# Kernel optimization log

Hardware: AMD Instinct MI355X
Metric: run time of the kernel (lower is better)

## Reference

```python
import jax, jax.numpy as jnp
import numpy as np

DEPTH = 3
DIM = 64
N_NODES = 4096
BATCH = 4


def setup_inputs() -> dict:
    key = jax.random.key(0)
    k1, k2, k3, k4 = jax.random.split(key, 4)
    x = jax.random.normal(k1, (BATCH, N_NODES, DIM), dtype=jnp.float32)
    graph = jax.random.uniform(k2, (BATCH, N_NODES, N_NODES), dtype=jnp.float32)
    # Linear((depth+1)*dim, dim): PyTorch default init U(-1/sqrt(fan_in), 1/sqrt(fan_in))
    fan_in = (DEPTH + 1) * DIM
    bound = 1.0 / np.sqrt(fan_in)
    W = jax.random.uniform(k3, (DIM, fan_in), minval=-bound, maxval=bound, dtype=jnp.float32)
    b = jax.random.uniform(k4, (DIM,), minval=-bound, maxval=bound, dtype=jnp.float32)
    return {"x": x, "graph": graph, "W": W, "b": b}


def reference(x, graph, W, b):
    # GCN branch of LocalGNN.forward (dropout p=0 -> identity).
    n = graph.shape[-1]
    g = graph + jnp.eye(n, dtype=graph.dtype)          # add self loops
    d = 1.0 / (jnp.sqrt(g.sum(axis=-1)) + 1e-7)        # [b, n]
    # D @ g @ D with D = diag(d):  g_ij * d_i * d_j
    g = g * d[..., :, None] * d[..., None, :]
    outs = [x]
    h = x
    for _ in range(DEPTH):
        h = jnp.einsum('bij,bjd->bid', g, h)           # dense propagation
        outs.append(h)
    cat = jnp.concatenate(outs, axis=-1)               # [b, n, (depth+1)*dim]
    return cat @ W.T + b
```

## Files before the change

### kernel.cpp

```cpp
#include <hip/hip_runtime.h>
#include <hip/hip_bf16.h>


typedef __attribute__((ext_vector_type(4))) float  floatx4;
typedef __attribute__((ext_vector_type(8))) short  short8;

#define NB 4
#define NN 4096
#define ND 64
#define HSZ ((size_t)NB * NN * ND)
#define HF_B 262144

__device__ __forceinline__ unsigned short f2bf_bits(float v) {
    __hip_bfloat16 b = __float2bfloat16(v);
    return *reinterpret_cast<unsigned short*>(&b);
}

__device__ __forceinline__ short8 pack8p(const float* v) {
    short8 r;
#pragma unroll
    for (int j = 0; j < 8; ++j) r[j] = (short)f2bf_bits(v[j]);
    return r;
}

__global__ void rowsum_kernel(const float* __restrict__ graph, float* __restrict__ dinv) {
    int row = blockIdx.x;
    const float* g = graph + (size_t)row * NN;
    int t = threadIdx.x;
    float s = 0.f;
#pragma unroll
    for (int q = 0; q < 4; ++q) {
        floatx4 v = *reinterpret_cast<const floatx4*>(g + q * 1024 + t * 4);
        s += v[0] + v[1] + v[2] + v[3];
    }
#pragma unroll
    for (int off = 32; off > 0; off >>= 1) s += __shfl_down(s, off);
    __shared__ float wsum[4];
    if ((t & 63) == 0) wsum[t >> 6] = s;
    __syncthreads();
    if (t == 0) {
        float tot = wsum[0] + wsum[1] + wsum[2] + wsum[3] + 1.0f;
        dinv[row] = 1.0f / (sqrtf(tot) + 1e-7f);
    }
}

__global__ __launch_bounds__(256) void make_ghat_sw(const float* __restrict__ g,
                                                    const float* __restrict__ dinv,
                                                    unsigned short* __restrict__ gsw) {
    __shared__ float tile[16][524];
    int bid = blockIdx.x;
    int b = bid >> 8, mt = bid & 255;
    int t = threadIdx.x;
    const float* grow  = g + ((size_t)b * NN + mt * 16) * NN;
    const float* dinvb = dinv + (size_t)b * NN;
    size_t outbase = (((size_t)(b * 256 + mt)) * 128) * 512;

    for (int s0 = 0; s0 < NN; s0 += 512) {
        __syncthreads();
#pragma unroll
        for (int li = 0; li < 8; ++li) {
            int flat = li * 1024 + t * 4;
            int r = flat >> 9, cidx = flat & 511;
            floatx4 v = *reinterpret_cast<const floatx4*>(grow + (size_t)r * NN + s0 + cidx);
            *reinterpret_cast<floatx4*>(&tile[r][cidx]) = v;
        }
        __syncthreads();
#pragma unroll
        for (int gg = 0; gg < 4; ++gg) {
            int gi = gg * 256 + t;
            int kcl = gi >> 6;
            int ln  = gi & 63;
            int m = ln & 15, q = ln >> 4;
            int i_row = mt * 16 + m;
            float di = dinvb[i_row];
            int kbase = s0 + kcl * 32 + q * 8;
            floatx4 dj0 = *reinterpret_cast<const floatx4*>(dinvb + kbase);
            floatx4 dj1 = *reinterpret_cast<const floatx4*>(dinvb + kbase + 4);
            float v[8];
#pragma unroll
            for (int j = 0; j < 8; ++j) {
                float xv = tile[m][kcl * 32 + q * 8 + j];
                if (kbase + j == i_row) xv += 1.0f;
                float dj = (j < 4) ? dj0[j] : dj1[j - 4];
                v[j] = xv * di * dj;
            }
            short8 o = pack8p(v);
            size_t kc = (size_t)(s0 >> 5) + kcl;
            *reinterpret_cast<short8*>(gsw + outbase + kc * 512 + ln * 8) = o;
        }
    }
}

__global__ void castF_kernel(const float* __restrict__ x, unsigned short* __restrict__ hF) {
    __shared__ float tile[64][65];
    int b = blockIdx.y, row0 = blockIdx.x * 64;
    size_t base = ((size_t)b * NN + row0) * ND;
    int t = threadIdx.x;
#pragma unroll
    for (int qi = 0; qi < 16; ++qi) {
        int idx = qi * 256 + t;
        tile[idx >> 6][idx & 63] = x[base + idx];
    }
    __syncthreads();
#pragma unroll
    for (int gg = 0; gg < 2; ++gg) {
        int gi = gg * 256 + t;
        int kcl = gi >> 8;
        int c   = (gi >> 6) & 3;
        int ln  = gi & 63;
        int m = ln & 15, q = ln >> 4;
        float v[8];
#pragma unroll
        for (int j = 0; j < 8; ++j) v[j] = tile[kcl * 32 + q * 8 + j][c * 16 + m];
        short8 o = pack8p(v);
        size_t kc = (size_t)blockIdx.x * 2 + kcl;
        *reinterpret_cast<short8*>(hF + (size_t)b * HF_B + ((kc * 4 + c) * 64 + ln) * 8) = o;
    }
}

__global__ __launch_bounds__(256, 4) void prop_gemm(const unsigned short* __restrict__ gsw,
                                                    const unsigned short* __restrict__ hF,
                                                    float* __restrict__ P) {
    int wid  = blockIdx.x * 4 + (threadIdx.x >> 6);
    int lane = threadIdx.x & 63;
    int b  = wid >> 10;
    int ks = (wid >> 8) & 3;
    int mt = wid & 255;
    int m = lane & 15, q = lane >> 4;

    const unsigned short* Ap = gsw + (((size_t)(b * 256 + mt)) * 128 + ks * 32) * 512 + lane * 8;
    const unsigned short* Bp = hF + (size_t)b * HF_B + (size_t)(ks * 32) * 2048 + lane * 8;

    floatx4 acc0 = {0.f,0.f,0.f,0.f}, acc1 = acc0, acc2 = acc0, acc3 = acc0;

#pragma unroll 2
    for (int kc = 0; kc < 32; ++kc) {
        short8 a  = *reinterpret_cast<const short8*>(Ap);
        short8 b0 = *reinterpret_cast<const short8*>(Bp);
        short8 b1 = *reinterpret_cast<const short8*>(Bp + 512);
        short8 b2 = *reinterpret_cast<const short8*>(Bp + 1024);
        short8 b3 = *reinterpret_cast<const short8*>(Bp + 1536);
        Ap += 512;
        Bp += 2048;
        acc0 = __builtin_amdgcn_mfma_f32_16x16x32_bf16(a, b0, acc0, 0, 0, 0);
        acc1 = __builtin_amdgcn_mfma_f32_16x16x32_bf16(a, b1, acc1, 0, 0, 0);
        acc2 = __builtin_amdgcn_mfma_f32_16x16x32_bf16(a, b2, acc2, 0, 0, 0);
        acc3 = __builtin_amdgcn_mfma_f32_16x16x32_bf16(a, b3, acc3, 0, 0, 0);
    }

    float* pout = P + ((size_t)ks * NB + b) * ((size_t)NN * ND);
    int row0 = mt * 16;
    floatx4* accs[4] = {&acc0, &acc1, &acc2, &acc3};
#pragma unroll
    for (int c = 0; c < 4; ++c)
#pragma unroll
        for (int r = 0; r < 4; ++r) {
            int row = row0 + q * 4 + r;
            pout[(size_t)row * ND + c * 16 + m] = (*accs[c])[r];
        }
}

__global__ void prep_kernel(const float* __restrict__ P,
                            unsigned short* __restrict__ hrow,
                            unsigned short* __restrict__ hF) {
    __shared__ float tile[64][65];
    int b = blockIdx.y, row0 = blockIdx.x * 64;
    size_t base = ((size_t)b * NN + row0) * ND;
    const size_t SZ = HSZ;
    int t = threadIdx.x;
#pragma unroll
    for (int qi = 0; qi < 16; ++qi) {
        int idx = qi * 256 + t;
        int r = idx >> 6, n = idx & 63;
        size_t off = base + idx;
        float s = P[off] + P[SZ + off] + P[2 * SZ + off] + P[3 * SZ + off];
        hrow[off] = f2bf_bits(s);
        tile[r][n] = s;
    }
    __syncthreads();
#pragma unroll
    for (int gg = 0; gg < 2; ++gg) {
        int gi = gg * 256 + t;
        int kcl = gi >> 8;
        int c   = (gi >> 6) & 3;
        int ln  = gi & 63;
        int m = ln & 15, q = ln >> 4;
        float v[8];
#pragma unroll
        for (int j = 0; j < 8; ++j) v[j] = tile[kcl * 32 + q * 8 + j][c * 16 + m];
        short8 o = pack8p(v);
        size_t kc = (size_t)blockIdx.x * 2 + kcl;
        *reinterpret_cast<short8*>(hF + (size_t)b * HF_B + ((kc * 4 + c) * 64 + ln) * 8) = o;
    }
}

__global__ __launch_bounds__(256) void final_linear(const float* __restrict__ x,
                                                    const unsigned short* __restrict__ h1,
                                                    const unsigned short* __restrict__ h2,
                                                    const unsigned short* __restrict__ h3,
                                                    const float* __restrict__ W,
                                                    const float* __restrict__ bias,
                                                    float* __restrict__ out) {
    int wid  = blockIdx.x * 4 + (threadIdx.x >> 6);
    int lane = threadIdx.x & 63;
    int b = wid >> 8;
    int row0 = (wid & 255) * 16;
    int m = lane & 15, q = lane >> 4;

    floatx4 acc[4];
#pragma unroll
    for (int c = 0; c < 4; ++c) acc[c] = (floatx4){0.f, 0.f, 0.f, 0.f};

    {
        const float* A = x + ((size_t)b * NN + row0 + m) * ND;
#pragma unroll
        for (int ki = 0; ki < 2; ++ki) {
            float av[8];
#pragma unroll
            for (int j = 0; j < 8; ++j) av[j] = A[ki * 32 + q * 8 + j];
            short8 af = pack8p(av);
#pragma unroll
            for (int c = 0; c < 4; ++c) {
                const float* Wr = W + (size_t)(c * 16 + m) * 256 + ki * 32 + q * 8;
                float wv[8];
#pragma unroll
                for (int j = 0; j < 8; ++j) wv[j] = Wr[j];
                short8 bf = pack8p(wv);
                acc[c] = __builtin_amdgcn_mfma_f32_16x16x32_bf16(af, bf, acc[c], 0, 0, 0);
            }
        }
    }
    const unsigned short* hs[3] = {h1, h2, h3};
#pragma unroll
    for (int p = 1; p < 4; ++p) {
        const unsigned short* A = hs[p - 1] + ((size_t)b * NN + row0 + m) * ND;
#pragma unroll
        for (int ki = 0; ki < 2; ++ki) {
            short8 af = *reinterpret_cast<const short8*>(A + ki * 32 + q * 8);
#pragma unroll
            for (int c = 0; c < 4; ++c) {
                const float* Wr = W + (size_t)(c * 16 + m) * 256 + p * 64 + ki * 32 + q * 8;
                float wv[8];
#pragma unroll
                for (int j = 0; j < 8; ++j) wv[j] = Wr[j];
                short8 bf = pack8p(wv);
                acc[c] = __builtin_amdgcn_mfma_f32_16x16x32_bf16(af, bf, acc[c], 0, 0, 0);
            }
        }
    }
#pragma unroll
    for (int c = 0; c < 4; ++c) {
        float bb = bias[c * 16 + m];
#pragma unroll
        for (int r = 0; r < 4; ++r) {
            int row = row0 + q * 4 + r;
            out[((size_t)b * NN + row) * ND + c * 16 + m] = acc[c][r] + bb;
        }
    }
}

extern "C" void kernel_launch(void* const* d_in, const int* in_sizes, int n_in,
                              void* d_out, int out_size, void* d_ws, size_t ws_size,
                              hipStream_t stream) {
    const float* x     = (const float*)d_in[0];
    const float* graph = (const float*)d_in[1];
    const float* W     = (const float*)d_in[2];
    const float* bias  = (const float*)d_in[3];
    float* out = (float*)d_out;

    char* w = (char*)d_ws;
    float*          dinv = (float*)w;
    unsigned short* hF   = (unsigned short*)(w + (1 << 16));
    unsigned short* gsw  = (unsigned short*)(w + (1 << 16) + (1 << 21));
    char* w2 = w + (1 << 16) + (1 << 21) + ((size_t)NB * NN * NN * 2);
    float*          P    = (float*)w2;
    unsigned short* h1   = (unsigned short*)(w2 + 4 * HSZ * 4);
    unsigned short* h2   = h1 + HSZ;
    unsigned short* h3   = h2 + HSZ;

    rowsum_kernel<<<NB * NN, 256, 0, stream>>>(graph, dinv);
    make_ghat_sw<<<NB * 256, 256, 0, stream>>>(graph, dinv, gsw);
    castF_kernel<<<dim3(NN / 64, NB), 256, 0, stream>>>(x, hF);

    unsigned short* houts[3] = {h1, h2, h3};
    for (int s = 0; s < 3; ++s) {
        prop_gemm<<<1024, 256, 0, stream>>>(gsw, hF, P);
        prep_kernel<<<dim3(NN / 64, NB), 256, 0, stream>>>(P, houts[s], hF);
    }
    final_linear<<<256, 256, 0, stream>>>(x, h1, h2, h3, W, bias, out);
}
```

Measured before the change: 591.4 us.

## Fuse rowsum into graph prep, apply D scaling to features, fuse split-K reduction and final linear

Rowsum and graph swizzling are merged into one pass that reads the graph once, storing the unnormalised (g+I) in bf16 and folding the D^-1/2 scaling onto the feature vectors instead. The propagation GEMM now reduces its split-K partials in shared memory within a block and writes bf16 outputs directly, removing the fp32 partial buffer and the separate prep kernels. The last propagation is fused with the final linear layer, and W is pre-swizzled to bf16 once. Kernel count drops from nine to four, at the cost of fewer blocks per GEMM launch and extra shared-memory syncs.

Measured after the change: 498.5 us. 1.19x faster.

```diff
diff --git a/kernel.cpp b/kernel.cpp
--- a/kernel.cpp
+++ b/kernel.cpp
@@ -8,14 +8,16 @@
 #define NB 4
 #define NN 4096
 #define ND 64
-#define HSZ ((size_t)NB * NN * ND)
 #define HF_B 262144
 
 __device__ __forceinline__ unsigned short f2bf_bits(float v) {
     __hip_bfloat16 b = __float2bfloat16(v);
     return *reinterpret_cast<unsigned short*>(&b);
 }
-
+__device__ __forceinline__ float bf2f(unsigned short u) {
+    unsigned int x = ((unsigned int)u) << 16;
+    return *reinterpret_cast<float*>(&x);
+}
 __device__ __forceinline__ short8 pack8p(const float* v) {
     short8 r;
 #pragma unroll
@@ -23,238 +25,239 @@
     return r;
 }
 
-__global__ void rowsum_kernel(const float* __restrict__ graph, float* __restrict__ dinv) {
-    int row = blockIdx.x;
-    const float* g = graph + (size_t)row * NN;
+__global__ __launch_bounds__(256) void prep_graph(const float* __restrict__ g,
+                                                  const float* __restrict__ x,
+                                                  const float* __restrict__ W,
+                                                  float* __restrict__ dinv,
+                                                  unsigned short* __restrict__ gswz,
+                                                  unsigned short* __restrict__ hF0,
+                                                  unsigned short* __restrict__ Wf) {
+    __shared__ float tile[16][516];
+    __shared__ float dl[16];
+    int tt = blockIdx.x;
+    int b = tt >> 8, mt = tt & 255;
     int t = threadIdx.x;
-    float s = 0.f;
-#pragma unroll
-    for (int q = 0; q < 4; ++q) {
-        floatx4 v = *reinterpret_cast<const floatx4*>(g + q * 1024 + t * 4);
-        s += v[0] + v[1] + v[2] + v[3];
-    }
-#pragma unroll
-    for (int off = 32; off > 0; off >>= 1) s += __shfl_down(s, off);
-    __shared__ float wsum[4];
-    if ((t & 63) == 0) wsum[t >> 6] = s;
-    __syncthreads();
-    if (t == 0) {
-        float tot = wsum[0] + wsum[1] + wsum[2] + wsum[3] + 1.0f;
-        dinv[row] = 1.0f / (sqrtf(tot) + 1e-7f);
-    }
-}
-
-__global__ __launch_bounds__(256) void make_ghat_sw(const float* __restrict__ g,
-                                                    const float* __restrict__ dinv,
-                                                    unsigned short* __restrict__ gsw) {
-    __shared__ float tile[16][524];
-    int bid = blockIdx.x;
-    int b = bid >> 8, mt = bid & 255;
-    int t = threadIdx.x;
-    const float* grow  = g + ((size_t)b * NN + mt * 16) * NN;
-    const float* dinvb = dinv + (size_t)b * NN;
-    size_t outbase = (((size_t)(b * 256 + mt)) * 128) * 512;
+    const float* grow = g + ((size_t)b * NN + mt * 16) * NN;
+    size_t outbase = (size_t)tt * 128 * 512;
+    float rs = 0.f;
 
     for (int s0 = 0; s0 < NN; s0 += 512) {
         __syncthreads();
 #pragma unroll
-        for (int li = 0; li < 8; ++li) {
-            int flat = li * 1024 + t * 4;
-            int r = flat >> 9, cidx = flat & 511;
-            floatx4 v = *reinterpret_cast<const floatx4*>(grow + (size_t)r * NN + s0 + cidx);
-            *reinterpret_cast<floatx4*>(&tile[r][cidx]) = v;
+        for (int it = 0; it < 8; ++it) {
+            int f4 = it * 256 + t;
+            int r = f4 >> 7, c4 = f4 & 127;
+            floatx4 v = *reinterpret_cast<const floatx4*>(grow + (size_t)r * NN + s0 + c4 * 4);
+            *reinterpret_cast<floatx4*>(&tile[r][c4 * 4]) = v;
         }
         __syncthreads();
+        {
+            int r = t >> 4, c0 = t & 15;
+            float s = 0.f;
+#pragma unroll
+            for (int j2 = 0; j2 < 32; ++j2) s += tile[r][c0 + j2 * 16];
+            rs += s;
+        }
 #pragma unroll
         for (int gg = 0; gg < 4; ++gg) {
             int gi = gg * 256 + t;
             int kcl = gi >> 6;
-            int ln  = gi & 63;
+            int ln = gi & 63;
             int m = ln & 15, q = ln >> 4;
             int i_row = mt * 16 + m;
-            float di = dinvb[i_row];
             int kbase = s0 + kcl * 32 + q * 8;
-            floatx4 dj0 = *reinterpret_cast<const floatx4*>(dinvb + kbase);
-            floatx4 dj1 = *reinterpret_cast<const floatx4*>(dinvb + kbase + 4);
             float v[8];
 #pragma unroll
             for (int j = 0; j < 8; ++j) {
                 float xv = tile[m][kcl * 32 + q * 8 + j];
                 if (kbase + j == i_row) xv += 1.0f;
-                float dj = (j < 4) ? dj0[j] : dj1[j - 4];
-                v[j] = xv * di * dj;
+                v[j] = xv;
             }
-            short8 o = pack8p(v);
-            size_t kc = (size_t)(s0 >> 5) + kcl;
-            *reinterpret_cast<short8*>(gsw + outbase + kc * 512 + ln * 8) = o;
-        }
-    }
-}
-
-__global__ void castF_kernel(const float* __restrict__ x, unsigned short* __restrict__ hF) {
-    __shared__ float tile[64][65];
-    int b = blockIdx.y, row0 = blockIdx.x * 64;
-    size_t base = ((size_t)b * NN + row0) * ND;
-    int t = threadIdx.x;
-#pragma unroll
-    for (int qi = 0; qi < 16; ++qi) {
-        int idx = qi * 256 + t;
-        tile[idx >> 6][idx & 63] = x[base + idx];
+            *reinterpret_cast<short8*>(gswz + outbase + ((size_t)((s0 >> 5) + kcl)) * 512 + ln * 8) = pack8p(v);
+        }
+    }
+#pragma unroll
+    for (int off = 8; off > 0; off >>= 1) rs += __shfl_down(rs, off, 16);
+    if ((t & 15) == 0) {
+        int r = t >> 4;
+        float d = 1.0f / (sqrtf(rs + 1.0f) + 1e-7f);
+        dinv[b * NN + mt * 16 + r] = d;
+        dl[r] = d;
     }
     __syncthreads();
-#pragma unroll
-    for (int gg = 0; gg < 2; ++gg) {
-        int gi = gg * 256 + t;
-        int kcl = gi >> 8;
-        int c   = (gi >> 6) & 3;
-        int ln  = gi & 63;
-        int m = ln & 15, q = ln >> 4;
+    {
+        const float* xp = x + ((size_t)b * NN + mt * 16) * ND;
+#pragma unroll
+        for (int e = 0; e < 4; ++e) {
+            int idx = e * 256 + t;
+            tile[idx >> 6][idx & 63] = xp[idx];
+        }
+    }
+    __syncthreads();
+    if (t < 128) {
+        int c = t >> 5, lnl = t & 31;
+        int q_loc = lnl >> 4, m = lnl & 15;
+        int u = mt & 1;
+        int ln = u * 32 + lnl;
+        int kc = mt >> 1;
         float v[8];
 #pragma unroll
-        for (int j = 0; j < 8; ++j) v[j] = tile[kcl * 32 + q * 8 + j][c * 16 + m];
-        short8 o = pack8p(v);
-        size_t kc = (size_t)blockIdx.x * 2 + kcl;
-        *reinterpret_cast<short8*>(hF + (size_t)b * HF_B + ((kc * 4 + c) * 64 + ln) * 8) = o;
-    }
-}
-
-__global__ __launch_bounds__(256, 4) void prop_gemm(const unsigned short* __restrict__ gsw,
-                                                    const unsigned short* __restrict__ hF,
-                                                    float* __restrict__ P) {
-    int wid  = blockIdx.x * 4 + (threadIdx.x >> 6);
-    int lane = threadIdx.x & 63;
-    int b  = wid >> 10;
-    int ks = (wid >> 8) & 3;
-    int mt = wid & 255;
-    int m = lane & 15, q = lane >> 4;
-
-    const unsigned short* Ap = gsw + (((size_t)(b * 256 + mt)) * 128 + ks * 32) * 512 + lane * 8;
-    const unsigned short* Bp = hF + (size_t)b * HF_B + (size_t)(ks * 32) * 2048 + lane * 8;
-
-    floatx4 acc0 = {0.f,0.f,0.f,0.f}, acc1 = acc0, acc2 = acc0, acc3 = acc0;
-
-#pragma unroll 2
-    for (int kc = 0; kc < 32; ++kc) {
-        short8 a  = *reinterpret_cast<const short8*>(Ap);
-        short8 b0 = *reinterpret_cast<const short8*>(Bp);
-        short8 b1 = *reinterpret_cast<const short8*>(Bp + 512);
-        short8 b2 = *reinterpret_cast<const short8*>(Bp + 1024);
-        short8 b3 = *reinterpret_cast<const short8*>(Bp + 1536);
-        Ap += 512;
-        Bp += 2048;
-        acc0 = __builtin_amdgcn_mfma_f32_16x16x32_bf16(a, b0, acc0, 0, 0, 0);
-        acc1 = __builtin_amdgcn_mfma_f32_16x16x32_bf16(a, b1, acc1, 0, 0, 0);
-        acc2 = __builtin_amdgcn_mfma_f32_16x16x32_bf16(a, b2, acc2, 0, 0, 0);
-        acc3 = __builtin_amdgcn_mfma_f32_16x16x32_bf16(a, b3, acc3, 0, 0, 0);
-    }
-
-    float* pout = P + ((size_t)ks * NB + b) * ((size_t)NN * ND);
-    int row0 = mt * 16;
-    floatx4* accs[4] = {&acc0, &acc1, &acc2, &acc3};
-#pragma unroll
-    for (int c = 0; c < 4; ++c)
-#pragma unroll
-        for (int r = 0; r < 4; ++r) {
-            int row = row0 + q * 4 + r;
-            pout[(size_t)row * ND + c * 16 + m] = (*accs[c])[r];
-        }
-}
-
-__global__ void prep_kernel(const float* __restrict__ P,
-                            unsigned short* __restrict__ hrow,
-                            unsigned short* __restrict__ hF) {
-    __shared__ float tile[64][65];
-    int b = blockIdx.y, row0 = blockIdx.x * 64;
-    size_t base = ((size_t)b * NN + row0) * ND;
-    const size_t SZ = HSZ;
-    int t = threadIdx.x;
-#pragma unroll
-    for (int qi = 0; qi < 16; ++qi) {
-        int idx = qi * 256 + t;
-        int r = idx >> 6, n = idx & 63;
-        size_t off = base + idx;
-        float s = P[off] + P[SZ + off] + P[2 * SZ + off] + P[3 * SZ + off];
-        hrow[off] = f2bf_bits(s);
-        tile[r][n] = s;
-    }
+        for (int j = 0; j < 8; ++j) {
+            int lr = q_loc * 8 + j;
+            v[j] = dl[lr] * tile[lr][c * 16 + m];
+        }
+        *reinterpret_cast<short8*>(hF0 + (size_t)b * HF_B + ((size_t)(kc * 4 + c) * 64 + ln) * 8) = pack8p(v);
+    }
+    if (tt == 0) {
+#pragma unroll
+        for (int e = 0; e < 8; ++e) {
+            int wi = e * 256 + t;
+            int kc = wi >> 8;
+            int c = (wi >> 6) & 3;
+            int ln = wi & 63;
+            int m = ln & 15, q = ln >> 4;
+            float v[8];
+#pragma unroll
+            for (int j = 0; j < 8; ++j) v[j] = W[(size_t)(c * 16 + m) * 256 + kc * 32 + q * 8 + j];
+            *reinterpret_cast<short8*>(Wf + ((size_t)(kc * 4 + c) * 64 + ln) * 8) = pack8p(v);
+        }
+    }
+}
+
+#define PROP_MAIN()                                                                      \
+    int bid = blockIdx.x;                                                                \
+    int b = bid >> 7, mk = bid & 127;                                                    \
+    int t = threadIdx.x;                                                                 \
+    int w = t >> 6, lane = t & 63;                                                       \
+    int m = lane & 15, q = lane >> 4;                                                    \
+    int tt0 = b * 256 + mk * 2;                                                          \
+    const unsigned short* Ap0 = gswz + ((size_t)tt0 * 128 + w * 32) * 512 + lane * 8;    \
+    const unsigned short* Ap1 = Ap0 + (size_t)128 * 512;                                 \
+    const unsigned short* Bp  = hFin + (size_t)b * HF_B + (size_t)(w * 32) * 2048 + lane * 8; \
+    floatx4 acc0[4], acc1[4];                                                            \
+    _Pragma("unroll")                                                                    \
+    for (int c = 0; c < 4; ++c) { acc0[c] = (floatx4){0.f,0.f,0.f,0.f}; acc1[c] = acc0[c]; } \
+    _Pragma("unroll 2")                                                                  \
+    for (int kc = 0; kc < 32; ++kc) {                                                    \
+        short8 a0 = *reinterpret_cast<const short8*>(Ap0);                               \
+        short8 a1 = *reinterpret_cast<const short8*>(Ap1);                               \
+        short8 b0 = *reinterpret_cast<const short8*>(Bp);                                \
+        short8 b1 = *reinterpret_cast<const short8*>(Bp + 512);                          \
+        short8 b2 = *reinterpret_cast<const short8*>(Bp + 1024);                         \
+        short8 b3 = *reinterpret_cast<const short8*>(Bp + 1536);                         \
+        Ap0 += 512; Ap1 += 512; Bp += 2048;                                              \
+        acc0[0] = __builtin_amdgcn_mfma_f32_16x16x32_bf16(a0, b0, acc0[0], 0, 0, 0);     \
+        acc1[0] = __builtin_amdgcn_mfma_f32_16x16x32_bf16(a1, b0, acc1[0], 0, 0, 0);     \
+        acc0[1] = __builtin_amdgcn_mfma_f32_16x16x32_bf16(a0, b1, acc0[1], 0, 0, 0);     \
+        acc1[1] = __builtin_amdgcn_mfma_f32_16x16x32_bf16(a1, b1, acc1[1], 0, 0, 0);     \
+        acc0[2] = __builtin_amdgcn_mfma_f32_16x16x32_bf16(a0, b2, acc0[2], 0, 0, 0);     \
+        acc1[2] = __builtin_amdgcn_mfma_f32_16x16x32_bf16(a1, b2, acc1[2], 0, 0, 0);     \
+        acc0[3] = __builtin_amdgcn_mfma_f32_16x16x32_bf16(a0, b3, acc0[3], 0, 0, 0);     \
+        acc1[3] = __builtin_amdgcn_mfma_f32_16x16x32_bf16(a1, b3, acc1[3], 0, 0, 0);     \
+    }                                                                                    \
+    if (t < 32) dl[t] = dinv[b * NN + mk * 32 + t];                                      \
+    for (int u = 0; u < 2; ++u) {                                                        \
+        __syncthreads();                                                                 \
+        floatx4* acc = u ? acc1 : acc0;                                                  \
+        _Pragma("unroll")                                                                \
+        for (int c = 0; c < 4; ++c)                                                      \
+            _Pragma("unroll")                                                            \
+            for (int r = 0; r < 4; ++r) buf[w][q * 4 + r][c * 16 + m] = acc[c][r];       \
+        __syncthreads();                                                                 \
+        _Pragma("unroll")                                                                \
+        for (int e = 0; e < 4; ++e) {                                                    \
+            int idx = e * 256 + t;                                                       \
+            int r = idx >> 6, col = idx & 63;                                            \
+            float s = buf[0][r][col] + buf[1][r][col] + buf[2][r][col] + buf[3][r][col]; \
+            int lr = u * 16 + r;                                                         \
+            hsh[lr][col] = f2bf_bits(dl[lr] * s);                                        \
+        }                                                                                \
+    }                                                                                    \
     __syncthreads();
-#pragma unroll
-    for (int gg = 0; gg < 2; ++gg) {
-        int gi = gg * 256 + t;
-        int kcl = gi >> 8;
-        int c   = (gi >> 6) & 3;
-        int ln  = gi & 63;
-        int m = ln & 15, q = ln >> 4;
+
+__global__ __launch_bounds__(256) void prop_pass(const unsigned short* __restrict__ gswz,
+                                                 const unsigned short* __restrict__ hFin,
+                                                 const float* __restrict__ dinv,
+                                                 unsigned short* __restrict__ hrow,
+                                                 unsigned short* __restrict__ hFout) {
+    __shared__ float buf[4][16][68];
+    __shared__ unsigned short hsh[32][64];
+    __shared__ float dl[32];
+    PROP_MAIN()
+    {
+        unsigned short* hp = hrow + ((size_t)b * NN + mk * 32) * ND;
+#pragma unroll
+        for (int e = 0; e < 8; ++e) {
+            int idx = e * 256 + t;
+            hp[idx] = hsh[idx >> 6][idx & 63];
+        }
+    }
+    {
+        int c = t >> 6, ln = t & 63;
+        int mm = ln & 15, qq = ln >> 4;
         float v[8];
 #pragma unroll
-        for (int j = 0; j < 8; ++j) v[j] = tile[kcl * 32 + q * 8 + j][c * 16 + m];
-        short8 o = pack8p(v);
-        size_t kc = (size_t)blockIdx.x * 2 + kcl;
-        *reinterpret_cast<short8*>(hF + (size_t)b * HF_B + ((kc * 4 + c) * 64 + ln) * 8) = o;
-    }
-}
-
-__global__ __launch_bounds__(256) void final_linear(const float* __restrict__ x,
-                                                    const unsigned short* __restrict__ h1,
-                                                    const unsigned short* __restrict__ h2,
-                                                    const unsigned short* __restrict__ h3,
-                                                    const float* __restrict__ W,
-                                                    const float* __restrict__ bias,
-                                                    float* __restrict__ out) {
-    int wid  = blockIdx.x * 4 + (threadIdx.x >> 6);
-    int lane = threadIdx.x & 63;
-    int b = wid >> 8;
-    int row0 = (wid & 255) * 16;
-    int m = lane & 15, q = lane >> 4;
-
-    floatx4 acc[4];
-#pragma unroll
-    for (int c = 0; c < 4; ++c) acc[c] = (floatx4){0.f, 0.f, 0.f, 0.f};
-
-    {
-        const float* A = x + ((size_t)b * NN + row0 + m) * ND;
-#pragma unroll
-        for (int ki = 0; ki < 2; ++ki) {
-            float av[8];
-#pragma unroll
-            for (int j = 0; j < 8; ++j) av[j] = A[ki * 32 + q * 8 + j];
-            short8 af = pack8p(av);
-#pragma unroll
-            for (int c = 0; c < 4; ++c) {
-                const float* Wr = W + (size_t)(c * 16 + m) * 256 + ki * 32 + q * 8;
-                float wv[8];
-#pragma unroll
-                for (int j = 0; j < 8; ++j) wv[j] = Wr[j];
-                short8 bf = pack8p(wv);
-                acc[c] = __builtin_amdgcn_mfma_f32_16x16x32_bf16(af, bf, acc[c], 0, 0, 0);
+        for (int j = 0; j < 8; ++j) {
+            int lr = qq * 8 + j;
+            v[j] = dl[lr] * bf2f(hsh[lr][c * 16 + mm]);
+        }
+        *reinterpret_cast<short8*>(hFout + (size_t)b * HF_B + ((size_t)(mk * 4 + c) * 64 + ln) * 8) = pack8p(v);
+    }
+}
+
+__global__ __launch_bounds__(256) void prop_final(const unsigned short* __restrict__ gswz,
+                                                  const unsigned short* __restrict__ hFin,
+                                                  const float* __restrict__ dinv,
+                                                  const float* __restrict__ x,
+                                                  const unsigned short* __restrict__ hrow1,
+                                                  const unsigned short* __restrict__ hrow2,
+                                                  const unsigned short* __restrict__ Wf,
+                                                  const float* __restrict__ bias,
+                                                  float* __restrict__ out) {
+    __shared__ float buf[4][16][68];
+    __shared__ unsigned short hsh[32][64];
+    __shared__ float dl[32];
+    PROP_MAIN()
+    if (w < 2) {
+        int u = w;
+        int grow = b * NN + mk * 32 + u * 16 + m;
+        floatx4 facc[4];
+#pragma unroll
+        for (int c = 0; c < 4; ++c) facc[c] = (floatx4){0.f, 0.f, 0.f, 0.f};
+#pragma unroll
+        for (int p = 0; p < 4; ++p) {
+#pragma unroll
+            for (int ki = 0; ki < 2; ++ki) {
+                short8 af;
+                if (p == 0) {
+                    const float* xp = x + (size_t)grow * ND + ki * 32 + q * 8;
+                    float v[8];
+#pragma unroll
+                    for (int j = 0; j < 8; ++j) v[j] = xp[j];
+                    af = pack8p(v);
+                } else if (p == 1) {
+                    af = *reinterpret_cast<const short8*>(hrow1 + (size_t)grow * ND + ki * 32 + q * 8);
+                } else if (p == 2) {
+                    af = *reinterpret_cast<const short8*>(hrow2 + (size_t)grow * ND + ki * 32 + q * 8);
+                } else {
+                    af = *reinterpret_cast<const short8*>(&hsh[u * 16 + m][ki * 32 + q * 8]);
+                }
+                int kc = p * 2 + ki;
+#pragma unroll
+                for (int c = 0; c < 4; ++c) {
+                    short8 bf = *reinterpret_cast<const short8*>(Wf + ((size_t)(kc * 4 + c) * 64 + lane) * 8);
+                    facc[c] = __builtin_amdgcn_mfma_f32_16x16x32_bf16(af, bf, facc[c], 0, 0, 0);
+                }
             }
         }
-    }
-    const unsigned short* hs[3] = {h1, h2, h3};
-#pragma unroll
-    for (int p = 1; p < 4; ++p) {
-        const unsigned short* A = hs[p - 1] + ((size_t)b * NN + row0 + m) * ND;
-#pragma unroll
-        for (int ki = 0; ki < 2; ++ki) {
-            short8 af = *reinterpret_cast<const short8*>(A + ki * 32 + q * 8);
-#pragma unroll
-            for (int c = 0; c < 4; ++c) {
-                const float* Wr = W + (size_t)(c * 16 + m) * 256 + p * 64 + ki * 32 + q * 8;
-                float wv[8];
-#pragma unroll
-                for (int j = 0; j < 8; ++j) wv[j] = Wr[j];
-                short8 bf = pack8p(wv);
-                acc[c] = __builtin_amdgcn_mfma_f32_16x16x32_bf16(af, bf, acc[c], 0, 0, 0);
+#pragma unroll
+        for (int c = 0; c < 4; ++c) {
+            float bb = bias[c * 16 + m];
+#pragma unroll
+            for (int r = 0; r < 4; ++r) {
+                int row = b * NN + mk * 32 + u * 16 + q * 4 + r;
+                out[(size_t)row * ND + c * 16 + m] = facc[c][r] + bb;
             }
-        }
-    }
-#pragma unroll
-    for (int c = 0; c < 4; ++c) {
-        float bb = bias[c * 16 + m];
-#pragma unroll
-        for (int r = 0; r < 4; ++r) {
-            int row = row0 + q * 4 + r;
-            out[((size_t)b * NN + row) * ND + c * 16 + m] = acc[c][r] + bb;
         }
     }
 }
@@ -269,23 +272,16 @@
     float* out = (float*)d_out;
 
     char* w = (char*)d_ws;
-    float*          dinv = (float*)w;
-    unsigned short* hF   = (unsigned short*)(w + (1 << 16));
-    unsigned short* gsw  = (unsigned short*)(w + (1 << 16) + (1 << 21));
-    char* w2 = w + (1 << 16) + (1 << 21) + ((size_t)NB * NN * NN * 2);
-    float*          P    = (float*)w2;
-    unsigned short* h1   = (unsigned short*)(w2 + 4 * HSZ * 4);
-    unsigned short* h2   = h1 + HSZ;
-    unsigned short* h3   = h2 + HSZ;
-
-    rowsum_kernel<<<NB * NN, 256, 0, stream>>>(graph, dinv);
-    make_ghat_sw<<<NB * 256, 256, 0, stream>>>(graph, dinv, gsw);
-    castF_kernel<<<dim3(NN / 64, NB), 256, 0, stream>>>(x, hF);
-
-    unsigned short* houts[3] = {h1, h2, h3};
-    for (int s = 0; s < 3; ++s) {
-        prop_gemm<<<1024, 256, 0, stream>>>(gsw, hF, P);
-        prep_kernel<<<dim3(NN / 64, NB), 256, 0, stream>>>(P, houts[s], hF);
-    }
-    final_linear<<<256, 256, 0, stream>>>(x, h1, h2, h3, W, bias, out);
-}
+    float*          dinv  = (float*)w;
+    unsigned short* Wf    = (unsigned short*)(w + (1 << 16));
+    unsigned short* hFa   = (unsigned short*)(w + (1 << 17));
+    unsigned short* hFb   = hFa + (size_t)NB * HF_B;
+    unsigned short* hrow1 = hFb + (size_t)NB * HF_B;
+    unsigned short* hrow2 = hrow1 + (size_t)NB * NN * ND;
+    unsigned short* gswz  = hrow2 + (size_t)NB * NN * ND;
+
+    prep_graph<<<1024, 256, 0, stream>>>(graph, x, W, dinv, gswz, hFa, Wf);
+    prop_pass<<<512, 256, 0, stream>>>(gswz, hFa, dinv, hrow1, hFb);
+    prop_pass<<<512, 256, 0, stream>>>(gswz, hFb, dinv, hrow2, hFa);
+    prop_final<<<512, 256, 0, stream>>>(gswz, hFa, dinv, x, hrow1, hrow2, Wf, bias, out);
+}
```
